# Kernel tuning notes

Hardware: AMD Instinct MI355X
Metric: run time of the kernel (lower is better)

The kernel has to match this reference:

```python
import jax, jax.numpy as jnp
import numpy as np

N = 100000   # nodes
E = 3200000  # edges
CY = 128     # channels_y (signal length per node)
HID = 10     # hidden_channels
H = 2        # heads
C = 10       # out channels per head
BN_EPS = 1e-5


def _glorot(k, shape):
    lim = float(np.sqrt(6.0 / (shape[0] + shape[1])))
    return jax.random.uniform(k, shape, jnp.float32, -lim, lim)


def setup_inputs() -> dict:
    key = jax.random.key(0)
    ks = jax.random.split(key, 16)
    p = {}
    p["signal"] = jax.random.normal(ks[0], (N, CY), jnp.float32)
    p["edge_index"] = jax.random.randint(ks[1], (2, E), 0, N)
    p["edge_weight"] = jax.random.uniform(ks[2], (E,), jnp.float32)
    p["mask"] = jax.random.bernoulli(ks[3], 0.3, (N,))
    # mlp_in: Linear(CY,512) -> BatchNorm -> ReLU -> Linear(512,HID) (PyG MLP, plain_last)
    p["W1"] = _glorot(ks[4], (CY, 512)); p["b1"] = jnp.zeros((512,), jnp.float32)
    p["gamma"] = jnp.ones((512,), jnp.float32); p["beta"] = jnp.zeros((512,), jnp.float32)
    p["W2"] = _glorot(ks[5], (512, HID)); p["b2"] = jnp.zeros((HID,), jnp.float32)
    # GATv2Conv(HID, HID, heads=2, edge_dim=1, concat=True)
    p["Wl"] = _glorot(ks[6], (HID, H * C)); p["bl"] = jnp.zeros((H * C,), jnp.float32)
    p["Wr"] = _glorot(ks[7], (HID, H * C)); p["br"] = jnp.zeros((H * C,), jnp.float32)
    p["We"] = _glorot(ks[8], (1, H * C))              # lin_edge, no bias
    p["att"] = _glorot(ks[9], (H, C))                 # attention vector per head
    p["gat_bias"] = jnp.zeros((H * C,), jnp.float32)
    # mlp_out: MLP([20,512]) single layer, plain_last -> just Linear (dropout off in eval)
    p["W3"] = _glorot(ks[10], (H * C, 512)); p["b3"] = jnp.zeros((512,), jnp.float32)
    # out_linear: Linear(512, CY)
    p["W4"] = _glorot(ks[11], (512, CY)); p["b4"] = jnp.zeros((CY,), jnp.float32)
    return p


def _forward(signal, edge_index, edge_weight, mask,
             W1, b1, gamma, beta, W2, b2,
             Wl, bl, Wr, br, We, att, gat_bias,
             W3, b3, W4, b4):
    # node masking: (signal.T * ~mask).T
    x = signal * (~mask)[:, None].astype(signal.dtype)
    # mlp_in (eval mode: BN with running mean=0, var=1)
    x = x @ W1 + b1
    x = x * (gamma / jnp.sqrt(jnp.asarray(1.0 + BN_EPS, x.dtype))) + beta
    x = jax.nn.relu(x)
    x = x @ W2 + b2                                   # [N, HID]
    # GATv2Conv
    src, dst = edge_index[0], edge_index[1]
    xl = (x @ Wl + bl).reshape(N, H, C)               # source transform
    xr = (x @ Wr + br).reshape(N, H, C)               # target transform
    ea = (edge_weight[:, None] @ We).reshape(E, H, C)  # edge feature transform
    e = jax.nn.leaky_relu(xl[src] + xr[dst] + ea, 0.2)  # [E,H,C]
    alpha = jnp.einsum('ehc,hc->eh', e, att)          # [E,H]
    # segment softmax over incoming edges of each dst node
    m = jax.ops.segment_max(alpha, dst, num_segments=N)
    ex = jnp.exp(alpha - m[dst])
    den = jax.ops.segment_sum(ex, dst, num_segments=N)
    a = ex / (den[dst] + 1e-16)                       # [E,H]
    out = jax.ops.segment_sum(xl[src] * a[:, :, None], dst, num_segments=N)
    out = out.reshape(N, H * C) + gat_bias            # concat heads + bias
    # mlp_out (single plain-last layer) + out_linear
    out = out @ W3 + b3
    out = out @ W4 + b4
    return out


def reference(signal, edge_index, edge_weight, mask,
              W1, b1, gamma, beta, W2, b2,
              Wl, bl, Wr, br, We, att, gat_bias,
              W3, b3, W4, b4):
    return _forward(signal, edge_index, edge_weight, mask,
                    W1, b1, gamma, beta, W2, b2,
                    Wl, bl, Wr, br, We, att, gat_bias,
                    W3, b3, W4, b4)
```

## Files before the change

### kernel.cpp

```cpp
#include <hip/hip_runtime.h>
#include <hip/hip_bf16.h>

constexpr int NN = 100000;
constexpr int NE = 3200000;
constexpr int CYC = 128;
constexpr int NB = 1563;
constexpr int EBLK = 256;
constexpr int ECHUNK = NE / EBLK;
constexpr int MSCAN = NB * EBLK;
constexpr int CAP = 2432;
constexpr int NBLK_A = (NN + 63) / 64;

#define OFF_W1T    0u
#define OFF_W2T    131072u
#define OFF_B1E    147456u
#define OFF_SMALL  149504u
#define OFF_W34    151808u
#define OFF_B34    162048u
#define OFF_FLAGS  162560u
#define OFF_XLB    163840u
#define OFF_XR     6563840u
#define OFF_GH     14965248u
#define OFF_BB     16565760u
#define OFF_BS     16572160u
#define OFF_BIN    16573184u

#define SF_WLR 0
#define SF_BLR 400
#define SF_ATT 440
#define SF_WE  460
#define SF_GB  480
#define SF_B2  500

typedef __attribute__((ext_vector_type(8))) short bf16x8;
typedef __attribute__((ext_vector_type(4))) float f32x4;

__device__ __forceinline__ float bfu(unsigned short x) {
  return __uint_as_float(((unsigned)x) << 16);
}
__device__ __forceinline__ short f2bf(float f) {
  __hip_bfloat16 h = __float2bfloat16(f);
  return *reinterpret_cast<short*>(&h);
}
__device__ __forceinline__ float LD(const void* p, long i, int f32f) {
  return f32f ? ((const float*)p)[i] : bfu(((const unsigned short*)p)[i]);
}

__global__ __launch_bounds__(256) void kPrep(
    const void* __restrict__ W1, const void* __restrict__ b1,
    const void* __restrict__ gamma, const void* __restrict__ beta,
    const void* __restrict__ W2, const void* __restrict__ b2,
    const void* __restrict__ Wl, const void* __restrict__ bl,
    const void* __restrict__ Wr, const void* __restrict__ br,
    const void* __restrict__ We, const void* __restrict__ att,
    const void* __restrict__ gbias, const void* __restrict__ W3,
    const void* __restrict__ b3, const void* __restrict__ W4,
    const void* __restrict__ b4, const void* __restrict__ mask,
    int* __restrict__ flags,
    short* __restrict__ W1T, float* __restrict__ b1eff, short* __restrict__ W2T,
    float* __restrict__ smallf, float* __restrict__ W34, float* __restrict__ b34)
{
  __shared__ int sfl[2];
  int t = threadIdx.x;
  if (t < 64) {
    const unsigned short* W1u = (const unsigned short*)W1;
    const unsigned* masku = (const unsigned*)mask;
    int big = 0;
#pragma unroll
    for (int k = 0; k < 8; k++) {
      unsigned e = (W1u[t * 8 + k] >> 7) & 0xFF;
      if (e >= 170) big++;
    }
    int byt = 0;
#pragma unroll
    for (int k = 0; k < 4; k++) if (masku[t * 4 + k] & ~1u) byt = 1;
#pragma unroll
    for (int o = 1; o < 64; o <<= 1) {
      big += __shfl_xor(big, o);
      byt |= __shfl_xor(byt, o);
    }
    if (t == 0) {
      sfl[0] = (big >= 4) ? 1 : 0;
      sfl[1] = byt;
      if (blockIdx.x == 0) { flags[0] = sfl[0]; flags[1] = byt; }
    }
  }
  __syncthreads();
  const int f32f = sfl[0];

  int tid = blockIdx.x * 256 + t;
  const float rs = 0.999995000037f;
  if (tid < 65536) {
    int j = tid >> 7, k = tid & 127;
    float s = LD(gamma, j, f32f) * rs;
    W1T[j * 128 + k] = f2bf(LD(W1, k * 512 + j, f32f) * s);
    if (k == 0) b1eff[j] = LD(b1, j, f32f) * s + LD(beta, j, f32f);
  } else if (tid < 73728) {
    int i = tid - 65536;
    int c = i >> 9, k = i & 511;
    W2T[c * 512 + k] = (c < 10) ? f2bf(LD(W2, k * 10 + c, f32f)) : (short)0;
  } else if (tid < 114688) {
    int i = tid - 73728;
    int o = i >> 4, k0 = i & 15;
    int j = o >> 7, tt = o & 127;
    float acc = 0.f;
    for (int k = k0; k < 512; k += 16)
      acc += LD(W3, j * 512 + k, f32f) * LD(W4, k * 128 + tt, f32f);
#pragma unroll
    for (int o2 = 1; o2 < 16; o2 <<= 1) acc += __shfl_xor(acc, o2);
    if (k0 == 0) W34[o] = acc;
  } else if (tid < 116736) {
    int i = tid - 114688;
    int tt = i >> 4, k0 = i & 15;
    float acc = 0.f;
    for (int k = k0; k < 512; k += 16)
      acc += LD(b3, k, f32f) * LD(W4, k * 128 + tt, f32f);
#pragma unroll
    for (int o2 = 1; o2 < 16; o2 <<= 1) acc += __shfl_xor(acc, o2);
    if (k0 == 0) b34[tt] = acc + LD(b4, tt, f32f);
  } else if (tid < 117252) {
    int i = tid - 116736;
    if (i < 400) {
      int c = i / 40, o = i % 40;
      smallf[SF_WLR + i] = (o < 20) ? LD(Wl, c * 20 + o, f32f) : LD(Wr, c * 20 + (o - 20), f32f);
    } else if (i < 440) {
      int o = i - 400;
      smallf[SF_BLR + o] = (o < 20) ? LD(bl, o, f32f) : LD(br, o - 20, f32f);
    } else if (i < 460) {
      smallf[SF_ATT + (i - 440)] = LD(att, i - 440, f32f);
    } else if (i < 480) {
      smallf[SF_WE + (i - 460)] = LD(We, i - 460, f32f);
    } else if (i < 500) {
      smallf[SF_GB + (i - 480)] = LD(gbias, i - 480, f32f);
    } else {
      int c = i - 500;
      smallf[SF_B2 + c] = (c < 10) ? LD(b2, c, f32f) : 0.f;
    }
  }
}

__global__ __launch_bounds__(256, 2) void kA(
    const void* __restrict__ sig, const void* __restrict__ mask,
    const short* __restrict__ W1T, const float* __restrict__ b1eff,
    const short* __restrict__ W2T, const float* __restrict__ smallf,
    const int* __restrict__ flags,
    unsigned short* __restrict__ xlb, float* __restrict__ xr)
{
  __shared__ __align__(16) char sR1[17408];
  __shared__ short sH[4][32 * 136];
  __shared__ float sb1[512];
  __shared__ float sxh[64][12];
  __shared__ float sWlr[400];
  __shared__ float sblr[40];
  __shared__ float sb2[16];

  short (*sA)[136]        = (short (*)[136])sR1;
  float (*sxhp)[64][17]   = (float (*)[64][17])sR1;
  float (*sxlr)[40]       = (float (*)[40])sR1;

  const int f32f = flags[0];
  const int mk8  = flags[1];
  int t = threadIdx.x;
  int w = t >> 6, l = t & 63;
  int lrow = l & 15, quad = l >> 4;
  int row0 = blockIdx.x * 64;

  for (int i = t; i < 512; i += 256) sb1[i] = b1eff[i];
  for (int i = t; i < 400; i += 256) sWlr[i] = smallf[SF_WLR + i];
  if (t < 40) sblr[t] = smallf[SF_BLR + t];
  if (t < 16) sb2[t] = smallf[SF_B2 + t];

  bf16x8 zz = {0, 0, 0, 0, 0, 0, 0, 0};
#pragma unroll
  for (int k = 0; k < 4; k++) {
    int idx = t + k * 256;
    int row = idx >> 4, seg = idx & 15;
    int gr = row0 + row;
    int grc = gr < NN ? gr : NN - 1;
    bool mbit = mk8 ? (((const unsigned char*)mask)[grc] != 0)
                    : (((const int*)mask)[grc] != 0);
    bf16x8 v;
    if (mbit) {
      v = zz;
    } else if (f32f) {
      const float4* Sf = (const float4*)((const float*)sig + (size_t)grc * CYC) + seg * 2;
      float4 x0 = Sf[0], x1 = Sf[1];
      v[0] = f2bf(x0.x); v[1] = f2bf(x0.y); v[2] = f2bf(x0.z); v[3] = f2bf(x0.w);
      v[4] = f2bf(x1.x); v[5] = f2bf(x1.y); v[6] = f2bf(x1.z); v[7] = f2bf(x1.w);
    } else {
      v = ((const bf16x8*)((const unsigned short*)sig + (size_t)grc * CYC))[seg];
    }
    *(bf16x8*)&sA[row][seg * 8] = v;
  }
  __syncthreads();

  float bcol[8];
#pragma unroll
  for (int ct = 0; ct < 8; ct++) bcol[ct] = sb1[w * 128 + ct * 16 + lrow];

  f32x4 acc[4][8];
#pragma unroll
  for (int rf = 0; rf < 4; rf++)
#pragma unroll
    for (int ct = 0; ct < 8; ct++) acc[rf][ct] = (f32x4){0.f, 0.f, 0.f, 0.f};

  const bf16x8* Bp = (const bf16x8*)W1T;
  int bvbase = w * 2048 + lrow * 16 + quad;
#pragma unroll
  for (int kt = 0; kt < 4; kt++) {
    bf16x8 a0 = *(const bf16x8*)&sA[lrow][kt * 32 + quad * 8];
    bf16x8 a1 = *(const bf16x8*)&sA[16 + lrow][kt * 32 + quad * 8];
    bf16x8 a2f = *(const bf16x8*)&sA[32 + lrow][kt * 32 + quad * 8];
    bf16x8 a3 = *(const bf16x8*)&sA[48 + lrow][kt * 32 + quad * 8];
#pragma unroll
    for (int ct = 0; ct < 8; ct++) {
      bf16x8 bv = Bp[bvbase + ct * 256 + kt * 4];
      acc[0][ct] = __builtin_amdgcn_mfma_f32_16x16x32_bf16(a0, bv, acc[0][ct], 0, 0, 0);
      acc[1][ct] = __builtin_amdgcn_mfma_f32_16x16x32_bf16(a1, bv, acc[1][ct], 0, 0, 0);
      acc[2][ct] = __builtin_amdgcn_mfma_f32_16x16x32_bf16(a2f, bv, acc[2][ct], 0, 0, 0);
      acc[3][ct] = __builtin_amdgcn_mfma_f32_16x16x32_bf16(a3, bv, acc[3][ct], 0, 0, 0);
    }
  }
  __syncthreads();

  const bf16x8* B2p = (const bf16x8*)W2T;
  bf16x8 b2v[4];
#pragma unroll
  for (int kt2 = 0; kt2 < 4; kt2++) b2v[kt2] = B2p[lrow * 64 + w * 16 + kt2 * 4 + quad];

  short* hb = &sH[w][0];
#pragma unroll
  for (int hf = 0; hf < 2; hf++) {
#pragma unroll
    for (int rr = 0; rr < 2; rr++) {
      int rf = hf * 2 + rr;
#pragma unroll
      for (int ct = 0; ct < 8; ct++) {
        float bb = bcol[ct];
#pragma unroll
        for (int r = 0; r < 4; r++) {
          float vv = fmaxf(acc[rf][ct][r] + bb, 0.f);
          hb[(rr * 16 + quad * 4 + r) * 136 + ct * 16 + lrow] = f2bf(vv);
        }
      }
    }
    asm volatile("s_waitcnt lgkmcnt(0)" ::: "memory");

    f32x4 a2[2];
    a2[0] = (f32x4){0.f, 0.f, 0.f, 0.f};
    a2[1] = (f32x4){0.f, 0.f, 0.f, 0.f};
#pragma unroll
    for (int kt2 = 0; kt2 < 4; kt2++) {
      bf16x8 x0 = *(const bf16x8*)&hb[lrow * 136 + kt2 * 32 + quad * 8];
      bf16x8 x1 = *(const bf16x8*)&hb[(16 + lrow) * 136 + kt2 * 32 + quad * 8];
      a2[0] = __builtin_amdgcn_mfma_f32_16x16x32_bf16(x0, b2v[kt2], a2[0], 0, 0, 0);
      a2[1] = __builtin_amdgcn_mfma_f32_16x16x32_bf16(x1, b2v[kt2], a2[1], 0, 0, 0);
    }
#pragma unroll
    for (int f = 0; f < 2; f++)
#pragma unroll
      for (int r = 0; r < 4; r++)
        sxhp[w][hf * 32 + f * 16 + quad * 4 + r][lrow] = a2[f][r];
  }
  __syncthreads();

  for (int i = t; i < 640; i += 256) {
    int row = i / 10, c = i - row * 10;
    sxh[row][c] = sxhp[0][row][c] + sxhp[1][row][c] + sxhp[2][row][c] + sxhp[3][row][c] + sb2[c];
  }
  __syncthreads();

  for (int i = t; i < 2560; i += 256) {
    int row = i / 40, o = i - row * 40;
    float v = sblr[o];
#pragma unroll
    for (int c = 0; c < 10; c++) v += sxh[row][c] * sWlr[c * 40 + o];
    sxlr[row][o] = v;
  }
  __syncthreads();

  int nrows = NN - row0; if (nrows > 64) nrows = 64;
  unsigned* xlb32 = (unsigned*)xlb;
#pragma unroll
  for (int k = 0; k < 4; k++) {
    int i = t + k * 256;
    int row = i >> 4, p = i & 15;
    if (row < nrows) {
      int s0 = 2 * p, s1 = 2 * p + 1;
      float lo = (s0 < 10) ? sxlr[row][s0] : (s0 >= 16 && s0 < 26) ? sxlr[row][s0 - 6] : 0.f;
      float hi = (s1 < 10) ? sxlr[row][s1] : (s1 >= 16 && s1 < 26) ? sxlr[row][s1 - 6] : 0.f;
      unsigned u = (unsigned)(unsigned short)f2bf(lo) |
                   ((unsigned)(unsigned short)f2bf(hi) << 16);
      xlb32[(size_t)(row0 + row) * 16 + p] = u;
    }
  }
#pragma unroll
  for (int k = 0; k < 5; k++) {
    int i = t + k * 256;
    int row = i / 20, c = i - row * 20;
    if (row < nrows) xr[(size_t)(row0 + row) * 20 + c] = sxlr[row][20 + c];
  }
}

__global__ __launch_bounds__(256) void kB1(const int* __restrict__ ei,
                                           int* __restrict__ gh) {
  __shared__ int h[NB];
  int t = threadIdx.x, blk = blockIdx.x;
  for (int i = t; i < NB; i += 256) h[i] = 0;
  __syncthreads();
  const int* dst = ei + NE;
  int base = blk * ECHUNK, bend = base + ECHUNK;
  for (int i = base + t; i < bend; i += 256)
    atomicAdd(&h[dst[i] >> 6], 1);
  __syncthreads();
  for (int i = t; i < NB; i += 256) gh[i * EBLK + blk] = h[i];
}

__global__ __launch_bounds__(256) void kS1(const int* __restrict__ in,
                                           int* __restrict__ outx,
                                           int* __restrict__ bsum, int nelem) {
  __shared__ int sS[256];
  int t = threadIdx.x;
  int base = blockIdx.x * 2048 + t * 8;
  int d[8], tsum = 0;
#pragma unroll
  for (int k = 0; k < 8; k++) {
    d[k] = (base + k < nelem) ? in[base + k] : 0;
    tsum += d[k];
  }
  sS[t] = tsum;
  __syncthreads();
  for (int o = 1; o < 256; o <<= 1) {
    int v = (t >= o) ? sS[t - o] : 0;
    __syncthreads();
    sS[t] += v;
    __syncthreads();
  }
  int run = sS[t] - tsum;
#pragma unroll
  for (int k = 0; k < 8; k++) {
    if (base + k < nelem) outx[base + k] = run;
    run += d[k];
  }
  if (t == 255) bsum[blockIdx.x] = sS[255];
}

__global__ __launch_bounds__(256) void kS2(int* __restrict__ bsum, int nb) {
  __shared__ int sS[256];
  int t = threadIdx.x;
  int v = (t < nb) ? bsum[t] : 0;
  sS[t] = v;
  __syncthreads();
  for (int o = 1; o < 256; o <<= 1) {
    int u = (t >= o) ? sS[t - o] : 0;
    __syncthreads();
    sS[t] += u;
    __syncthreads();
  }
  if (t < nb) bsum[t] = sS[t] - v;
}

__global__ __launch_bounds__(256) void kS3(int* __restrict__ gh,
                                           const int* __restrict__ bsum,
                                           int* __restrict__ bb) {
  int i = blockIdx.x * 256 + threadIdx.x;
  int v = gh[i] + bsum[i >> 11];
  gh[i] = v;
  if ((i & 255) == 0) bb[i >> 8] = v;
  if (i == 0) bb[NB] = NE;
}

__global__ __launch_bounds__(256) void kB3(const int* __restrict__ ei,
                                           const void* __restrict__ ew,
                                           const int* __restrict__ flags,
                                           const int* __restrict__ gh,
                                           int2* __restrict__ binned) {
  __shared__ int cur[NB];
  const int f32f = flags[0];
  int t = threadIdx.x, blk = blockIdx.x;
  for (int i = t; i < NB; i += 256) cur[i] = gh[i * EBLK + blk];
  __syncthreads();
  int base = blk * ECHUNK, bend = base + ECHUNK;
  for (int i = base + t; i < bend; i += 256) {
    int s = ei[i], d = ei[NE + i];
    float w = LD(ew, i, f32f);
    int b = d >> 6;
    int pos = atomicAdd(&cur[b], 1);
    binned[pos] = make_int2(s | ((d & 63) << 17), __float_as_int(w));
  }
}

__global__ __launch_bounds__(512) void kAgg(
    const int* __restrict__ bb, const int2* __restrict__ binned,
    const unsigned short* __restrict__ xlb, const float* __restrict__ xr,
    const float* __restrict__ smallf, const float* __restrict__ W34,
    const float* __restrict__ b34, const int* __restrict__ flags,
    void* __restrict__ out)
{
  __shared__ int2  sES[CAP];
  __shared__ float sXr[64 * 20];
  __shared__ float sW[2560];
  __shared__ float sb[128];
  __shared__ int   sCnt[64], sPre[64], sStart[64], sCur[64];
  __shared__ float sAtt[20], sWe[20], sGb[20];

  const int f32f = flags[0];
  int t = threadIdx.x, b = blockIdx.x;
  int node0 = b * 64;

  for (int i = t; i < 2560; i += 512) sW[i] = W34[i];
  for (int i = t; i < 1280; i += 512) {
    int gi = node0 * 20 + i;
    sXr[i] = (gi < NN * 20) ? xr[gi] : 0.f;
  }
  if (t < 128) sb[t] = b34[t];
  if (t < 64) sCnt[t] = 0;
  if (t < 20) { sAtt[t] = smallf[SF_ATT + t]; sWe[t] = smallf[SF_WE + t]; sGb[t] = smallf[SF_GB + t]; }
  __syncthreads();

  int base = bb[b], end = bb[b + 1];
  int ne = end - base;

  for (int i = t; i < ne; i += 512)
    atomicAdd(&sCnt[(unsigned)binned[base + i].x >> 17], 1);
  __syncthreads();

  if (t < 64) sPre[t] = sCnt[t];
  __syncthreads();
  for (int o = 1; o < 64; o <<= 1) {
    int v = 0;
    if (t < 64 && t >= o) v = sPre[t - o];
    __syncthreads();
    if (t < 64) sPre[t] += v;
    __syncthreads();
  }
  if (t < 64) {
    int ex = sPre[t] - sCnt[t];
    sStart[t] = ex;
    sCur[t] = ex;
  }
  __syncthreads();

  for (int i = t; i < ne; i += 512) {
    int2 e = binned[base + i];
    int dl = (unsigned)e.x >> 17;
    int pos = atomicAdd(&sCur[dl], 1);
    if (pos < CAP) sES[pos] = make_int2(e.x & 0x1FFFF, e.y);
  }
  __syncthreads();

  int n = t >> 3, sub = t & 7, head = sub >> 2, part = sub & 3;
  float xrw[10], attw[10], wew[10];
#pragma unroll
  for (int c = 0; c < 10; c++) {
    xrw[c]  = sXr[n * 20 + head * 10 + c];
    attw[c] = sAtt[head * 10 + c];
    wew[c]  = sWe[head * 10 + c];
  }
  float acc[10];
#pragma unroll
  for (int c = 0; c < 10; c++) acc[c] = 0.f;
  float den = 0.f;
  int s0 = sStart[n];
  int s1 = s0 + sCnt[n];
  if (s1 > CAP) s1 = CAP;

  int i = s0 + part;
  int2 e; uint4 q; unsigned q4;
  if (i < s1) {
    e = sES[i];
    const unsigned short* p = xlb + (size_t)e.x * 32 + head * 16;
    q = *(const uint4*)p;
    q4 = *(const unsigned*)(p + 8);
  }
  while (i < s1) {
    int j = i + 4;
    int2 en; uint4 qn; unsigned qn4;
    if (j < s1) {
      en = sES[j];
      const unsigned short* pn = xlb + (size_t)en.x * 32 + head * 16;
      qn = *(const uint4*)pn;
      qn4 = *(const unsigned*)(pn + 8);
    }
    float vl[10];
    unsigned qq[5] = {q.x, q.y, q.z, q.w, q4};
#pragma unroll
    for (int k = 0; k < 5; k++) {
      vl[2 * k]     = __uint_as_float(qq[k] << 16);
      vl[2 * k + 1] = __uint_as_float(qq[k] & 0xffff0000u);
    }
    float ww = __int_as_float(e.y);
    float a = 0.f;
#pragma unroll
    for (int c = 0; c < 10; c++) {
      float v = vl[c] + xrw[c] + ww * wew[c];
      v = fmaxf(v, 0.2f * v);
      a += v * attw[c];
    }
    float pp = __expf(a);
    den += pp;
#pragma unroll
    for (int c = 0; c < 10; c++) acc[c] += pp * vl[c];
    e = en; q = qn; q4 = qn4; i = j;
  }
  den += __shfl_xor(den, 1);
  den += __shfl_xor(den, 2);
#pragma unroll
  for (int c = 0; c < 10; c++) {
    acc[c] += __shfl_xor(acc[c], 1);
    acc[c] += __shfl_xor(acc[c], 2);
  }

  __syncthreads();
  if (part == 0) {
    float inv = 1.f / (den + 1e-16f);
#pragma unroll
    for (int c = 0; c < 10; c++)
      sXr[n * 20 + head * 10 + c] = acc[c] * inv + sGb[head * 10 + c];
  }
  __syncthreads();

  int col = t & 127, grp = t >> 7;
  for (int n2 = grp; n2 < 64; n2 += 4) {
    int gn = node0 + n2;
    if (gn >= NN) break;
    float v = sb[col];
    const float* g = &sXr[n2 * 20];
#pragma unroll
    for (int c = 0; c < 20; c++) v += g[c] * sW[c * 128 + col];
    if (f32f) ((float*)out)[(size_t)gn * 128 + col] = v;
    else ((unsigned short*)out)[(size_t)gn * 128 + col] = (unsigned short)f2bf(v);
  }
}

extern "C" void kernel_launch(void* const* d_in, const int* in_sizes, int n_in,
                              void* d_out, int out_size, void* d_ws, size_t ws_size,
                              hipStream_t stream) {
  (void)in_sizes; (void)n_in; (void)out_size; (void)ws_size;
  const void* sig  = d_in[0];
  const int*  ei   = (const int*)d_in[1];
  const void* ew   = d_in[2];
  const void* mask = d_in[3];
  const void* W1   = d_in[4];
  const void* b1   = d_in[5];
  const void* gam  = d_in[6];
  const void* bet  = d_in[7];
  const void* W2   = d_in[8];
  const void* b2   = d_in[9];
  const void* Wl   = d_in[10];
  const void* bl   = d_in[11];
  const void* Wr   = d_in[12];
  const void* br   = d_in[13];
  const void* We   = d_in[14];
  const void* att  = d_in[15];
  const void* gb   = d_in[16];
  const void* W3   = d_in[17];
  const void* b3   = d_in[18];
  const void* W4   = d_in[19];
  const void* b4   = d_in[20];

  char* ws = (char*)d_ws;
  short* W1T    = (short*)(ws + OFF_W1T);
  short* W2T    = (short*)(ws + OFF_W2T);
  float* b1eff  = (float*)(ws + OFF_B1E);
  float* smallf = (float*)(ws + OFF_SMALL);
  float* W34    = (float*)(ws + OFF_W34);
  float* b34    = (float*)(ws + OFF_B34);
  int*   flags  = (int*)(ws + OFF_FLAGS);
  unsigned short* xlb = (unsigned short*)(ws + OFF_XLB);
  float* xr     = (float*)(ws + OFF_XR);
  int*   gh     = (int*)(ws + OFF_GH);
  int*   bb     = (int*)(ws + OFF_BB);
  int*   bsum   = (int*)(ws + OFF_BS);
  int2*  bincsr = (int2*)(ws + OFF_BIN);

  kPrep<<<459, 256, 0, stream>>>(W1, b1, gam, bet, W2, b2, Wl, bl, Wr, br, We, att,
                                 gb, W3, b3, W4, b4, mask, flags,
                                 W1T, b1eff, W2T, smallf, W34, b34);
  kA<<<NBLK_A, 256, 0, stream>>>(sig, mask, W1T, b1eff, W2T, smallf, flags, xlb, xr);
  kB1<<<EBLK, 256, 0, stream>>>(ei, gh);
  kS1<<<(MSCAN + 2047) / 2048, 256, 0, stream>>>(gh, gh, bsum, MSCAN);
  kS2<<<1, 256, 0, stream>>>(bsum, (MSCAN + 2047) / 2048);
  kS3<<<NB, 256, 0, stream>>>(gh, bsum, bb);
  kB3<<<EBLK, 256, 0, stream>>>(ei, ew, flags, gh, bincsr);
  kAgg<<<NB, 512, 0, stream>>>(bb, bincsr, xlb, xr, smallf, W34, b34, flags, d_out);
}
```

Before: 403.1 us.

## Fuse edge histogram into prep kernel and replace three-pass scan with atomic-offset bucket scan

The destination histogram is now computed by extra blocks appended to the prep kernel, and the three-kernel global prefix scan is replaced by per-bucket block scans that run as extra blocks in the MLP kernel. Each bucket reserves its base with an atomicAdd on a global counter. Bucket ranges therefore become non-contiguous and unordered, so explicit begin/end arrays are passed to the aggregation kernel. This cuts four launches and their serialization, at the cost of nondeterministic bucket placement and extra shared-memory aliasing in the MLP kernel.

After: 386.6 us. -4.1%, faster.

```diff
diff --git a/kernel.cpp b/kernel.cpp
--- a/kernel.cpp
+++ b/kernel.cpp
@@ -7,9 +7,9 @@
 constexpr int NB = 1563;
 constexpr int EBLK = 256;
 constexpr int ECHUNK = NE / EBLK;
-constexpr int MSCAN = NB * EBLK;
 constexpr int CAP = 2432;
 constexpr int NBLK_A = (NN + 63) / 64;
+constexpr int NPREP = 459;
 
 #define OFF_W1T    0u
 #define OFF_W2T    131072u
@@ -20,9 +20,10 @@
 #define OFF_FLAGS  162560u
 #define OFF_XLB    163840u
 #define OFF_XR     6563840u
+#define OFF_BE     14563840u
 #define OFF_GH     14965248u
 #define OFF_BB     16565760u
-#define OFF_BS     16572160u
+#define OFF_GC     16572160u
 #define OFF_BIN    16573184u
 
 #define SF_WLR 0
@@ -46,7 +47,7 @@
   return f32f ? ((const float*)p)[i] : bfu(((const unsigned short*)p)[i]);
 }
 
-__global__ __launch_bounds__(256) void kPrep(
+__global__ __launch_bounds__(256) void kPrepHist(
     const void* __restrict__ W1, const void* __restrict__ b1,
     const void* __restrict__ gamma, const void* __restrict__ beta,
     const void* __restrict__ W2, const void* __restrict__ b2,
@@ -56,12 +57,29 @@
     const void* __restrict__ gbias, const void* __restrict__ W3,
     const void* __restrict__ b3, const void* __restrict__ W4,
     const void* __restrict__ b4, const void* __restrict__ mask,
+    const int* __restrict__ ei,
     int* __restrict__ flags,
     short* __restrict__ W1T, float* __restrict__ b1eff, short* __restrict__ W2T,
-    float* __restrict__ smallf, float* __restrict__ W34, float* __restrict__ b34)
+    float* __restrict__ smallf, float* __restrict__ W34, float* __restrict__ b34,
+    int* __restrict__ gh, int* __restrict__ gcnt)
 {
+  __shared__ int h[NB];
   __shared__ int sfl[2];
   int t = threadIdx.x;
+
+  if (blockIdx.x >= NPREP) {
+    int blk = blockIdx.x - NPREP;
+    for (int i = t; i < NB; i += 256) h[i] = 0;
+    __syncthreads();
+    const int* dst = ei + NE;
+    int base = blk * ECHUNK, bend_ = base + ECHUNK;
+    for (int i = base + t; i < bend_; i += 256)
+      atomicAdd(&h[dst[i] >> 6], 1);
+    __syncthreads();
+    for (int i = t; i < NB; i += 256) gh[i * EBLK + blk] = h[i];
+    return;
+  }
+
   if (t < 64) {
     const unsigned short* W1u = (const unsigned short*)W1;
     const unsigned* masku = (const unsigned*)mask;
@@ -82,7 +100,7 @@
     if (t == 0) {
       sfl[0] = (big >= 4) ? 1 : 0;
       sfl[1] = byt;
-      if (blockIdx.x == 0) { flags[0] = sfl[0]; flags[1] = byt; }
+      if (blockIdx.x == 0) { flags[0] = sfl[0]; flags[1] = byt; gcnt[0] = 0; }
     }
   }
   __syncthreads();
@@ -139,12 +157,14 @@
   }
 }
 
-__global__ __launch_bounds__(256, 2) void kA(
+__global__ __launch_bounds__(256, 2) void kAScan(
     const void* __restrict__ sig, const void* __restrict__ mask,
     const short* __restrict__ W1T, const float* __restrict__ b1eff,
     const short* __restrict__ W2T, const float* __restrict__ smallf,
     const int* __restrict__ flags,
-    unsigned short* __restrict__ xlb, float* __restrict__ xr)
+    unsigned short* __restrict__ xlb, float* __restrict__ xr,
+    int* __restrict__ gh, int* __restrict__ bb, int* __restrict__ bend,
+    int* __restrict__ gcnt)
 {
   __shared__ __align__(16) char sR1[17408];
   __shared__ short sH[4][32 * 136];
@@ -158,9 +178,31 @@
   float (*sxhp)[64][17]   = (float (*)[64][17])sR1;
   float (*sxlr)[40]       = (float (*)[40])sR1;
 
+  int t = threadIdx.x;
+
+  if (blockIdx.x >= NBLK_A) {
+    int* sS = (int*)sb1;
+    int* sBase = (int*)sb2;
+    int b = blockIdx.x - NBLK_A;
+    int c = gh[b * EBLK + t];
+    sS[t] = c;
+    __syncthreads();
+    for (int o = 1; o < 256; o <<= 1) {
+      int v = (t >= o) ? sS[t - o] : 0;
+      __syncthreads();
+      sS[t] += v;
+      __syncthreads();
+    }
+    if (t == 255) sBase[0] = atomicAdd(gcnt, sS[255]);
+    __syncthreads();
+    int base = sBase[0];
+    gh[b * EBLK + t] = base + sS[t] - c;
+    if (t == 255) { bb[b] = base; bend[b] = base + sS[255]; }
+    return;
+  }
+
   const int f32f = flags[0];
   const int mk8  = flags[1];
-  int t = threadIdx.x;
   int w = t >> 6, l = t & 63;
   int lrow = l & 15, quad = l >> 4;
   int row0 = blockIdx.x * 64;
@@ -236,10 +278,10 @@
       int rf = hf * 2 + rr;
 #pragma unroll
       for (int ct = 0; ct < 8; ct++) {
-        float bb = bcol[ct];
+        float bb_ = bcol[ct];
 #pragma unroll
         for (int r = 0; r < 4; r++) {
-          float vv = fmaxf(acc[rf][ct][r] + bb, 0.f);
+          float vv = fmaxf(acc[rf][ct][r] + bb_, 0.f);
           hb[(rr * 16 + quad * 4 + r) * 136 + ct * 16 + lrow] = f2bf(vv);
         }
       }
@@ -302,74 +344,6 @@
   }
 }
 
-__global__ __launch_bounds__(256) void kB1(const int* __restrict__ ei,
-                                           int* __restrict__ gh) {
-  __shared__ int h[NB];
-  int t = threadIdx.x, blk = blockIdx.x;
-  for (int i = t; i < NB; i += 256) h[i] = 0;
-  __syncthreads();
-  const int* dst = ei + NE;
-  int base = blk * ECHUNK, bend = base + ECHUNK;
-  for (int i = base + t; i < bend; i += 256)
-    atomicAdd(&h[dst[i] >> 6], 1);
-  __syncthreads();
-  for (int i = t; i < NB; i += 256) gh[i * EBLK + blk] = h[i];
-}
-
-__global__ __launch_bounds__(256) void kS1(const int* __restrict__ in,
-                                           int* __restrict__ outx,
-                                           int* __restrict__ bsum, int nelem) {
-  __shared__ int sS[256];
-  int t = threadIdx.x;
-  int base = blockIdx.x * 2048 + t * 8;
-  int d[8], tsum = 0;
-#pragma unroll
-  for (int k = 0; k < 8; k++) {
-    d[k] = (base + k < nelem) ? in[base + k] : 0;
-    tsum += d[k];
-  }
-  sS[t] = tsum;
-  __syncthreads();
-  for (int o = 1; o < 256; o <<= 1) {
-    int v = (t >= o) ? sS[t - o] : 0;
-    __syncthreads();
-    sS[t] += v;
-    __syncthreads();
-  }
-  int run = sS[t] - tsum;
-#pragma unroll
-  for (int k = 0; k < 8; k++) {
-    if (base + k < nelem) outx[base + k] = run;
-    run += d[k];
-  }
-  if (t == 255) bsum[blockIdx.x] = sS[255];
-}
-
-__global__ __launch_bounds__(256) void kS2(int* __restrict__ bsum, int nb) {
-  __shared__ int sS[256];
-  int t = threadIdx.x;
-  int v = (t < nb) ? bsum[t] : 0;
-  sS[t] = v;
-  __syncthreads();
-  for (int o = 1; o < 256; o <<= 1) {
-    int u = (t >= o) ? sS[t - o] : 0;
-    __syncthreads();
-    sS[t] += u;
-    __syncthreads();
-  }
-  if (t < nb) bsum[t] = sS[t] - v;
-}
-
-__global__ __launch_bounds__(256) void kS3(int* __restrict__ gh,
-                                           const int* __restrict__ bsum,
-                                           int* __restrict__ bb) {
-  int i = blockIdx.x * 256 + threadIdx.x;
-  int v = gh[i] + bsum[i >> 11];
-  gh[i] = v;
-  if ((i & 255) == 0) bb[i >> 8] = v;
-  if (i == 0) bb[NB] = NE;
-}
-
 __global__ __launch_bounds__(256) void kB3(const int* __restrict__ ei,
                                            const void* __restrict__ ew,
                                            const int* __restrict__ flags,
@@ -380,8 +354,8 @@
   int t = threadIdx.x, blk = blockIdx.x;
   for (int i = t; i < NB; i += 256) cur[i] = gh[i * EBLK + blk];
   __syncthreads();
-  int base = blk * ECHUNK, bend = base + ECHUNK;
-  for (int i = base + t; i < bend; i += 256) {
+  int base = blk * ECHUNK, bend_ = base + ECHUNK;
+  for (int i = base + t; i < bend_; i += 256) {
     int s = ei[i], d = ei[NE + i];
     float w = LD(ew, i, f32f);
     int b = d >> 6;
@@ -391,7 +365,8 @@
 }
 
 __global__ __launch_bounds__(512) void kAgg(
-    const int* __restrict__ bb, const int2* __restrict__ binned,
+    const int* __restrict__ bb, const int* __restrict__ bend,
+    const int2* __restrict__ binned,
     const unsigned short* __restrict__ xlb, const float* __restrict__ xr,
     const float* __restrict__ smallf, const float* __restrict__ W34,
     const float* __restrict__ b34, const int* __restrict__ flags,
@@ -418,7 +393,7 @@
   if (t < 20) { sAtt[t] = smallf[SF_ATT + t]; sWe[t] = smallf[SF_WE + t]; sGb[t] = smallf[SF_GB + t]; }
   __syncthreads();
 
-  int base = bb[b], end = bb[b + 1];
+  int base = bb[b], end = bend[b];
   int ne = end - base;
 
   for (int i = t; i < ne; i += 512)
@@ -569,19 +544,17 @@
   int*   flags  = (int*)(ws + OFF_FLAGS);
   unsigned short* xlb = (unsigned short*)(ws + OFF_XLB);
   float* xr     = (float*)(ws + OFF_XR);
+  int*   bendp  = (int*)(ws + OFF_BE);
   int*   gh     = (int*)(ws + OFF_GH);
   int*   bb     = (int*)(ws + OFF_BB);
-  int*   bsum   = (int*)(ws + OFF_BS);
+  int*   gcnt   = (int*)(ws + OFF_GC);
   int2*  bincsr = (int2*)(ws + OFF_BIN);
 
-  kPrep<<<459, 256, 0, stream>>>(W1, b1, gam, bet, W2, b2, Wl, bl, Wr, br, We, att,
-                                 gb, W3, b3, W4, b4, mask, flags,
-                                 W1T, b1eff, W2T, smallf, W34, b34);
-  kA<<<NBLK_A, 256, 0, stream>>>(sig, mask, W1T, b1eff, W2T, smallf, flags, xlb, xr);
-  kB1<<<EBLK, 256, 0, stream>>>(ei, gh);
-  kS1<<<(MSCAN + 2047) / 2048, 256, 0, stream>>>(gh, gh, bsum, MSCAN);
-  kS2<<<1, 256, 0, stream>>>(bsum, (MSCAN + 2047) / 2048);
-  kS3<<<NB, 256, 0, stream>>>(gh, bsum, bb);
+  kPrepHist<<<NPREP + EBLK, 256, 0, stream>>>(
+      W1, b1, gam, bet, W2, b2, Wl, bl, Wr, br, We, att, gb, W3, b3, W4, b4,
+      mask, ei, flags, W1T, b1eff, W2T, smallf, W34, b34, gh, gcnt);
+  kAScan<<<NBLK_A + NB, 256, 0, stream>>>(
+      sig, mask, W1T, b1eff, W2T, smallf, flags, xlb, xr, gh, bb, bendp, gcnt);
   kB3<<<EBLK, 256, 0, stream>>>(ei, ew, flags, gh, bincsr);
-  kAgg<<<NB, 512, 0, stream>>>(bb, bincsr, xlb, xr, smallf, W34, b34, flags, d_out);
-}
+  kAgg<<<NB, 512, 0, stream>>>(bb, bendp, bincsr, xlb, xr, smallf, W34, b34, flags, d_out);
+}
```
